# Performance work log

Hardware: AMD Instinct MI355X
Metric: run time of the kernel (lower is better)

## Reference

```python
import jax, jax.numpy as jnp
import numpy as np

B, S, H, NH, L, INTER, WIN = 2, 2048, 512, 8, 4, 2048, 64
HD = H // NH
W1 = WIN // 2          # one-sided window
WB = 2 * W1 + 1        # band width per query
EPS = 1e-12


def layer_norm(x, g, b):
    m = jnp.mean(x, axis=-1, keepdims=True)
    v = jnp.var(x, axis=-1, keepdims=True)
    return (x - m) / jnp.sqrt(v + EPS) * g + b


def setup_inputs() -> dict:
    key = jax.random.key(0)
    ks = jax.random.split(key, 12)
    std = 0.02
    n = lambda k, sh: jax.random.normal(k, sh, jnp.float32) * std
    return {
        "input_embs": jax.random.normal(ks[0], (B, S, H), jnp.float32),
        "attention_mask": jnp.ones((B, S), jnp.float32),
        "pos_emb": n(ks[1], (S, H)),
        "ln_emb_g": jnp.ones((H,), jnp.float32),
        "ln_emb_b": jnp.zeros((H,), jnp.float32),
        "Wq": n(ks[2], (L, H, H)), "bq": jnp.zeros((L, H), jnp.float32),
        "Wk": n(ks[3], (L, H, H)), "bk": jnp.zeros((L, H), jnp.float32),
        "Wv": n(ks[4], (L, H, H)), "bv": jnp.zeros((L, H), jnp.float32),
        "Wo": n(ks[5], (L, H, H)), "bo": jnp.zeros((L, H), jnp.float32),
        "ln1_g": jnp.ones((L, H), jnp.float32), "ln1_b": jnp.zeros((L, H), jnp.float32),
        "Wi": n(ks[6], (L, H, INTER)), "bi": jnp.zeros((L, INTER), jnp.float32),
        "Wo2": n(ks[7], (L, INTER, H)), "bo2": jnp.zeros((L, H), jnp.float32),
        "ln2_g": jnp.ones((L, H), jnp.float32), "ln2_b": jnp.zeros((L, H), jnp.float32),
        "pool_W1": n(ks[8], (H, H)), "pool_b1": jnp.zeros((H,), jnp.float32),
        "pool_W2": n(ks[9], (H, 1)), "pool_b2": jnp.zeros((1,), jnp.float32),
    }


def reference(input_embs, attention_mask, pos_emb, ln_emb_g, ln_emb_b,
              Wq, bq, Wk, bk, Wv, bv, Wo, bo, ln1_g, ln1_b,
              Wi, bi, Wo2, bo2, ln2_g, ln2_b,
              pool_W1, pool_b1, pool_W2, pool_b2):
    # extended additive mask: 0 for attend, -10000 for pad (no global tokens)
    ext = (1.0 - attention_mask) * -10000.0          # [B,S]
    is_masked = ext < 0                              # masked query positions

    # embeddings: input + position, LayerNorm (dropout is identity in eval)
    x = layer_norm(input_embs + pos_emb[None], ln_emb_g, ln_emb_b)

    # sliding-window band indices
    offs = jnp.arange(-W1, W1 + 1)
    idx = jnp.arange(S)[:, None] + offs[None, :]     # [S,WB]
    valid = (idx >= 0) & (idx < S)
    idxc = jnp.clip(idx, 0, S - 1)
    key_bias = ext[:, idxc]                          # [B,S,WB] additive key mask
    scale = 1.0 / jnp.sqrt(jnp.float32(HD))

    def layer(h, p):
        (wq, bq_, wk, bk_, wv, bv_, wo, bo_, g1, b1,
         wi, bi_, wo2, bo2_, g2, b2) = p
        q = (h @ wq + bq_).reshape(B, S, NH, HD) * scale
        k = (h @ wk + bk_).reshape(B, S, NH, HD)
        v = (h @ wv + bv_).reshape(B, S, NH, HD)
        kb = k[:, idxc]                              # [B,S,WB,NH,HD]
        vb = v[:, idxc]
        sc = jnp.einsum('bshd,bswhd->bhsw', q, kb) + key_bias[:, None]
        sc = jnp.where(valid[None, None], sc, -jnp.inf)
        pr = jax.nn.softmax(sc, axis=-1)
        pr = jnp.where(is_masked[:, None, :, None], 0.0, pr)
        ctx = jnp.einsum('bhsw,bswhd->bshd', pr, vb).reshape(B, S, H)
        attn = layer_norm(ctx @ wo + bo_ + h, g1, b1)          # BertSelfOutput
        inter = jax.nn.gelu(attn @ wi + bi_, approximate=False)  # BertIntermediate
        out = layer_norm(inter @ wo2 + bo2_ + attn, g2, b2)      # BertOutput
        return out, None

    params = (Wq, bq, Wk, bk, Wv, bv, Wo, bo, ln1_g, ln1_b,
              Wi, bi, Wo2, bo2, ln2_g, ln2_b)
    x, _ = jax.lax.scan(jax.checkpoint(layer), x, params)

    # AttentionPooling
    e = jnp.tanh(x @ pool_W1 + pool_b1)
    alpha = jnp.exp(e @ pool_W2 + pool_b2) * attention_mask[..., None]  # [B,S,1]
    alpha = alpha / (jnp.sum(alpha, axis=1, keepdims=True) + 1e-8)
    return jnp.einsum('bsh,bs->bh', x, alpha[..., 0])  # [B,H]
```

## Files before the change

kernel.cpp:

```cpp
#include <hip/hip_runtime.h>
#include <hip/hip_bf16.h>
#include <math.h>

#define B_ 2
#define S_ 2048
#define H_ 512
#define NH_ 8
#define HD_ 64
#define L_ 4
#define INTER_ 2048
#define W1_ 32
#define WB_ 65
#define M_ (B_*S_)

typedef __attribute__((ext_vector_type(8))) short short8v;
typedef __attribute__((ext_vector_type(4))) float f32x4;

__device__ __forceinline__ float b2f(ushort u){ return __uint_as_float(((unsigned)u)<<16); }
__device__ __forceinline__ ushort f2b(float f){
  unsigned u = __float_as_uint(f);
  unsigned r = (u + 0x7fffu + ((u>>16)&1u)) >> 16;
  return (ushort)r;
}

__device__ __forceinline__ void async16(const ushort* g, ushort* l){
  __builtin_amdgcn_global_load_lds(
      (const __attribute__((address_space(1))) unsigned int*)g,
      (__attribute__((address_space(3))) unsigned int*)l, 16, 0, 0);
}

__global__ __launch_bounds__(256) void transpose_k(const float* __restrict__ src,
    ushort* __restrict__ dst, int R, int C, size_t sBatch, size_t dBatch)
{
  __shared__ ushort tile[32][33];
  src += (size_t)blockIdx.z * sBatch;
  dst += (size_t)blockIdx.z * dBatch;
  int tx = threadIdx.x & 31, ty = threadIdx.x >> 5;
  int r0 = blockIdx.y * 32, c0 = blockIdx.x * 32;
  #pragma unroll
  for (int i = 0; i < 4; ++i){
    int r = r0 + ty + i*8;
    tile[ty + i*8][tx] = f2b(src[(size_t)r * C + c0 + tx]);
  }
  __syncthreads();
  #pragma unroll
  for (int i = 0; i < 4; ++i){
    int c = c0 + ty + i*8;
    dst[(size_t)c * R + r0 + tx] = tile[tx][ty + i*8];
  }
}

__global__ __launch_bounds__(256) void pack_bqkv(const float* __restrict__ bq,
    const float* __restrict__ bk, const float* __restrict__ bv, float* __restrict__ dst)
{
  int i = blockIdx.x * 256 + threadIdx.x;
  int l = i / 1536, n = i % 1536;
  float v = (n < 512) ? bq[l*512 + n] : (n < 1024 ? bk[l*512 + n - 512] : bv[l*512 + n - 1024]);
  dst[i] = v;
}

template<int EPI, int BM>
__global__ __launch_bounds__(256, (BM == 64) ? 4 : 3) void gemm_bt(
    const ushort* __restrict__ A, const ushort* __restrict__ Bt,
    const float* __restrict__ bias, ushort* __restrict__ o16,
    float* __restrict__ o32, int M, int N, int K, int Klen)
{
  constexpr int ABUF = BM * 32;
  constexpr int BUFE = ABUF + 4096;
  constexpr int MI = BM / 32;
  constexpr int AL = BM / 64;
  __shared__ ushort lds[3 * BUFE];
  const int tid = threadIdx.x;
  const int bm = blockIdx.y * BM, bn = blockIdx.x * 128;
  const int kbeg = blockIdx.z * Klen;
  const int wave = tid >> 6, lane = tid & 63;
  const int wr = (wave >> 1) * (BM / 2), wc = (wave & 1) * 64;
  const int lr = lane & 15, lg = lane >> 4;
  const int lkS = (lg ^ ((lr >> 1) & 3)) * 8;
  f32x4 acc[MI][4] = {};

  const int srow = tid >> 2;
  const int schk = (((tid & 3) ^ ((tid >> 3) & 3))) * 8;
  const ushort* Ag  = A  + (size_t)(bm + srow) * K + kbeg + schk;
  const ushort* Bg0 = Bt + (size_t)(bn + srow) * K + kbeg + schk;
  const ushort* Bg1 = Bt + (size_t)(bn + 64 + srow) * K + kbeg + schk;

  const int nIter = Klen >> 5;
  auto issueTile = [&](int t, int buf){
    int k0 = t << 5;
    ushort* d = &lds[0] + buf*BUFE + tid*8;
    #pragma unroll
    for (int r = 0; r < AL; ++r)
      async16(Ag + (size_t)r*64*K + k0, d + r*2048);
    async16(Bg0 + k0, d + ABUF);
    async16(Bg1 + k0, d + ABUF + 2048);
  };

  issueTile(0, 0);
  issueTile(1, 1);

  int cb = 0;
  for (int t = 0; t < nIter; ++t){
    int ib = cb + 2; if (ib >= 3) ib -= 3;
    if (t + 2 < nIter) issueTile(t + 2, ib);
    if constexpr (BM == 64){
      if (t + 2 < nIter)      asm volatile("s_waitcnt vmcnt(6)" ::: "memory");
      else if (t + 1 < nIter) asm volatile("s_waitcnt vmcnt(3)" ::: "memory");
      else                    asm volatile("s_waitcnt vmcnt(0)" ::: "memory");
    } else {
      if (t + 2 < nIter)      asm volatile("s_waitcnt vmcnt(8)" ::: "memory");
      else if (t + 1 < nIter) asm volatile("s_waitcnt vmcnt(4)" ::: "memory");
      else                    asm volatile("s_waitcnt vmcnt(0)" ::: "memory");
    }
    __builtin_amdgcn_sched_barrier(0);
    __builtin_amdgcn_s_barrier();
    const ushort* bufp = &lds[0] + cb*BUFE;
    short8v af[MI], bfr[4];
    #pragma unroll
    for (int mi = 0; mi < MI; ++mi)
      af[mi] = *(const short8v*)(bufp + (wr + mi*16 + lr)*32 + lkS);
    #pragma unroll
    for (int nj = 0; nj < 4; ++nj)
      bfr[nj] = *(const short8v*)(bufp + ABUF + (wc + nj*16 + lr)*32 + lkS);
    #pragma unroll
    for (int mi = 0; mi < MI; ++mi)
      #pragma unroll
      for (int nj = 0; nj < 4; ++nj)
        acc[mi][nj] = __builtin_amdgcn_mfma_f32_16x16x32_bf16(af[mi], bfr[nj], acc[mi][nj], 0, 0, 0);
    __builtin_amdgcn_s_barrier();
    cb = cb + 1; if (cb == 3) cb = 0;
  }

  const float bscale = (blockIdx.z == 0) ? 1.0f : 0.0f;
  #pragma unroll
  for (int mi = 0; mi < MI; ++mi){
    #pragma unroll
    for (int nj = 0; nj < 4; ++nj){
      int col = bn + wc + nj*16 + lr;
      float bv = bias[col] * bscale;
      #pragma unroll
      for (int j = 0; j < 4; ++j){
        int row = bm + wr + mi*16 + lg*4 + j;
        float v = acc[mi][nj][j] + bv;
        if (EPI == 1) v = 0.5f * v * (1.0f + erff(v * 0.70710678118654752f));
        if (EPI == 2) v = tanhf(v);
        if (EPI == 3) o32[(size_t)blockIdx.z*M*N + (size_t)row * N + col] = v;
        else          o16[(size_t)row * N + col] = f2b(v);
      }
    }
  }
}

__device__ __forceinline__ void block_ln_stats(float v0, float v1, float* red,
                                               float& mean, float& rstd)
{
  int tid = threadIdx.x, wave = tid >> 6, lane = tid & 63;
  float sm = v0 + v1;
  float sq = v0*v0 + v1*v1;
  #pragma unroll
  for (int o = 32; o > 0; o >>= 1){ sm += __shfl_xor(sm, o); sq += __shfl_xor(sq, o); }
  if (lane == 0){ red[wave] = sm; red[4 + wave] = sq; }
  __syncthreads();
  float S = red[0] + red[1] + red[2] + red[3];
  float Q = red[4] + red[5] + red[6] + red[7];
  mean = S * (1.0f / 512.0f);
  float var = Q * (1.0f / 512.0f) - mean*mean;
  if (var < 0.f) var = 0.f;
  rstd = rsqrtf(var + 1e-12f);
}

__global__ __launch_bounds__(256) void embed_ln(const float* __restrict__ x,
    const float* __restrict__ pos, const float* __restrict__ g,
    const float* __restrict__ bb, ushort* __restrict__ out16, float* __restrict__ out32)
{
  __shared__ float red[8];
  int row = blockIdx.x, tid = threadIdx.x;
  int s = row & (S_ - 1);
  const size_t base = (size_t)row*H_ + tid*2;
  float2 xv = *(const float2*)(x + base);
  float2 pv = *(const float2*)(pos + (size_t)s*H_ + tid*2);
  float v0 = xv.x + pv.x, v1 = xv.y + pv.y;
  float mean, rstd;
  block_ln_stats(v0, v1, red, mean, rstd);
  float2 gv = *(const float2*)(g + tid*2);
  float2 bv = *(const float2*)(bb + tid*2);
  float r0 = (v0 - mean)*rstd*gv.x + bv.x;
  float r1 = (v1 - mean)*rstd*gv.y + bv.y;
  ushort2 o2; o2.x = f2b(r0); o2.y = f2b(r1);
  *(ushort2*)(out16 + base) = o2;
  float2 f2v; f2v.x = r0; f2v.y = r1;
  *(float2*)(out32 + base) = f2v;
}

__global__ __launch_bounds__(256) void ln_res(const float* __restrict__ t,
    const float* __restrict__ res, const float* __restrict__ g,
    const float* __restrict__ bb, ushort* __restrict__ out16, float* __restrict__ out32)
{
  __shared__ float red[8];
  int row = blockIdx.x, tid = threadIdx.x;
  const size_t MN = (size_t)M_*H_;
  const size_t base = (size_t)row*H_ + tid*2;
  float2 t0 = *(const float2*)(t + base);
  float2 t1v = *(const float2*)(t + MN + base);
  float2 rv = *(const float2*)(res + base);
  float v0 = t0.x + t1v.x + rv.x;
  float v1 = t0.y + t1v.y + rv.y;
  float mean, rstd;
  block_ln_stats(v0, v1, red, mean, rstd);
  float2 gv = *(const float2*)(g + tid*2);
  float2 bv = *(const float2*)(bb + tid*2);
  float r0 = (v0 - mean)*rstd*gv.x + bv.x;
  float r1 = (v1 - mean)*rstd*gv.y + bv.y;
  ushort2 o2; o2.x = f2b(r0); o2.y = f2b(r1);
  *(ushort2*)(out16 + base) = o2;
  float2 f2v; f2v.x = r0; f2v.y = r1;
  *(float2*)(out32 + base) = f2v;
}

__global__ __launch_bounds__(256) void attn_mfma(const ushort* __restrict__ qkv,
    const float* __restrict__ mask, ushort* __restrict__ ctx)
{
  __shared__ ushort K_lds[128][72];
  __shared__ ushort Vt[64][136];
  __shared__ ushort P_lds[64][136];
  __shared__ float  kb[128];

  const int tid = threadIdx.x, wave = tid >> 6, lane = tid & 63;
  const int hh = blockIdx.y & (NH_ - 1), b = blockIdx.y >> 3;
  const int s0 = blockIdx.x * 64;
  const size_t rb = (size_t)b * S_;

  const int ch = tid & 7;
  const int rr = tid >> 3;
  #pragma unroll
  for (int it = 0; it < 4; ++it){
    int c = rr + it*32;
    int j = s0 - 32 + c;
    int jc = min(max(j, 0), S_ - 1);
    const size_t rowb = (rb + jc) * 1536 + hh*64 + ch*8;
    *(short8v*)(&K_lds[c][ch*8]) = *(const short8v*)(qkv + rowb + 512);
    short8v vv = *(const short8v*)(qkv + rowb + 1024);
    #pragma unroll
    for (int t = 0; t < 8; ++t){
      int tt = (t + ch) & 7;
      Vt[ch*8 + tt][c] = (ushort)vv[tt];
    }
  }
  if (tid < 128){
    int j = s0 - 32 + tid;
    kb[tid] = (j >= 0 && j < S_) ? (1.0f - mask[rb + j]) * (-10000.0f) : -1e30f;
  }
  __syncthreads();

  const int wq0 = wave * 16;
  const int lr = lane & 15, lg = lane >> 4, lk = lg * 8;

  const ushort* qbase = qkv + (rb + s0 + wq0 + lr) * 1536 + hh*64;
  short8v aq0 = *(const short8v*)(qbase + lk);
  short8v aq1 = *(const short8v*)(qbase + 32 + lk);

  f32x4 sacc[8];
  #pragma unroll
  for (int cn = 0; cn < 8; ++cn){
    short8v bk0 = *(const short8v*)(&K_lds[cn*16 + lr][lk]);
    short8v bk1 = *(const short8v*)(&K_lds[cn*16 + lr][32 + lk]);
    f32x4 z = {0.f, 0.f, 0.f, 0.f};
    z = __builtin_amdgcn_mfma_f32_16x16x32_bf16(aq0, bk0, z, 0, 0, 0);
    z = __builtin_amdgcn_mfma_f32_16x16x32_bf16(aq1, bk1, z, 0, 0, 0);
    sacc[cn] = z;
  }

  #pragma unroll
  for (int jr = 0; jr < 4; ++jr){
    const int R = wq0 + lg*4 + jr;
    float v[8], mx = -1e30f;
    #pragma unroll
    for (int cn = 0; cn < 8; ++cn){
      int c = cn*16 + lr;
      float sc = sacc[cn][jr] * 0.125f + kb[c];
      if (c < R || c > R + 64) sc = -1e30f;
      v[cn] = sc;
      mx = fmaxf(mx, sc);
    }
    #pragma unroll
    for (int o = 1; o < 16; o <<= 1) mx = fmaxf(mx, __shfl_xor(mx, o));
    float sum = 0.f;
    #pragma unroll
    for (int cn = 0; cn < 8; ++cn){ v[cn] = __expf(v[cn] - mx); sum += v[cn]; }
    #pragma unroll
    for (int o = 1; o < 16; o <<= 1) sum += __shfl_xor(sum, o);
    float qm = mask[rb + s0 + R];
    float inv = ((qm < 0.999f) ? 0.0f : 1.0f) / sum;
    #pragma unroll
    for (int cn = 0; cn < 8; ++cn)
      P_lds[R][cn*16 + lr] = f2b(v[cn] * inv);
  }

  short8v ap[4];
  #pragma unroll
  for (int ks = 0; ks < 4; ++ks)
    ap[ks] = *(const short8v*)(&P_lds[wq0 + lr][ks*32 + lk]);
  #pragma unroll
  for (int dn = 0; dn < 4; ++dn){
    f32x4 z = {0.f, 0.f, 0.f, 0.f};
    #pragma unroll
    for (int ks = 0; ks < 4; ++ks){
      short8v bv = *(const short8v*)(&Vt[dn*16 + lr][ks*32 + lk]);
      z = __builtin_amdgcn_mfma_f32_16x16x32_bf16(ap[ks], bv, z, 0, 0, 0);
    }
    #pragma unroll
    for (int jr = 0; jr < 4; ++jr){
      int R = wq0 + lg*4 + jr;
      ctx[(rb + s0 + R)*H_ + hh*64 + dn*16 + lr] = f2b(z[jr]);
    }
  }
}

__global__ __launch_bounds__(256) void pool_logit(const ushort* __restrict__ e,
    const float* __restrict__ w2, const float* __restrict__ b2p,
    const float* __restrict__ mask, float* __restrict__ alpha)
{
  int tid = threadIdx.x, wave = tid >> 6, lane = tid & 63;
  int r = blockIdx.x * 4 + wave;
  short8v ev = *(const short8v*)(e + (size_t)r*H_ + lane*8);
  float sacc = 0.f;
  #pragma unroll
  for (int j = 0; j < 8; ++j) sacc += b2f((ushort)ev[j]) * w2[lane*8 + j];
  #pragma unroll
  for (int o = 32; o > 0; o >>= 1) sacc += __shfl_xor(sacc, o);
  if (lane == 0){
    float logit = sacc + b2p[0];
    alpha[r] = __expf(logit) * mask[r];
  }
}

__global__ __launch_bounds__(256) void pool_sum(const float* __restrict__ alpha,
                                                float* __restrict__ invsum)
{
  __shared__ float red[4];
  int b = blockIdx.x, tid = threadIdx.x, wave = tid >> 6, lane = tid & 63;
  float s = 0.f;
  for (int k = tid; k < S_; k += 256) s += alpha[b*S_ + k];
  #pragma unroll
  for (int o = 32; o > 0; o >>= 1) s += __shfl_xor(s, o);
  if (lane == 0) red[wave] = s;
  __syncthreads();
  if (tid == 0) invsum[b] = 1.0f / (red[0] + red[1] + red[2] + red[3] + 1e-8f);
}

__global__ __launch_bounds__(256) void pool_wsum(const float* __restrict__ x,
    const float* __restrict__ alpha, float* __restrict__ out_acc)
{
  int chunk = blockIdx.x, b = blockIdx.y, tid = threadIdx.x;
  int s0 = chunk * 128;
  int c0 = tid * 2;
  float a0 = 0.f, a1 = 0.f;
  for (int i = 0; i < 128; ++i){
    int srow = s0 + i;
    float al = alpha[b*S_ + srow];
    float2 xv = *(const float2*)(x + (size_t)(b*S_ + srow)*H_ + c0);
    a0 += xv.x * al;
    a1 += xv.y * al;
  }
  float2 o; o.x = a0; o.y = a1;
  *(float2*)(out_acc + (size_t)chunk*B_*H_ + b*H_ + c0) = o;
}

__global__ __launch_bounds__(256) void pool_final(const float* __restrict__ out_acc,
    const float* __restrict__ invsum, float* __restrict__ out)
{
  int i = blockIdx.x * 256 + threadIdx.x;
  if (i < B_*H_){
    int b = i >> 9;
    float s = 0.f;
    #pragma unroll
    for (int c = 0; c < 16; ++c) s += out_acc[(size_t)c*B_*H_ + i];
    out[i] = s * invsum[b];
  }
}

extern "C" void kernel_launch(void* const* d_in, const int* in_sizes, int n_in,
                              void* d_out, int out_size, void* d_ws, size_t ws_size,
                              hipStream_t stream)
{
  const float* input_embs = (const float*)d_in[0];
  const float* mask       = (const float*)d_in[1];
  const float* pos        = (const float*)d_in[2];
  const float* ln_emb_g   = (const float*)d_in[3];
  const float* ln_emb_b   = (const float*)d_in[4];
  const float* Wq  = (const float*)d_in[5];
  const float* bq  = (const float*)d_in[6];
  const float* Wk  = (const float*)d_in[7];
  const float* bk  = (const float*)d_in[8];
  const float* Wv  = (const float*)d_in[9];
  const float* bv  = (const float*)d_in[10];
  const float* Wo  = (const float*)d_in[11];
  const float* bo  = (const float*)d_in[12];
  const float* ln1_g = (const float*)d_in[13];
  const float* ln1_b = (const float*)d_in[14];
  const float* Wi  = (const float*)d_in[15];
  const float* bi  = (const float*)d_in[16];
  const float* Wo2 = (const float*)d_in[17];
  const float* bo2 = (const float*)d_in[18];
  const float* ln2_g = (const float*)d_in[19];
  const float* ln2_b = (const float*)d_in[20];
  const float* pW1 = (const float*)d_in[21];
  const float* pb1 = (const float*)d_in[22];
  const float* pW2 = (const float*)d_in[23];
  const float* pb2 = (const float*)d_in[24];

  char* ws = (char*)d_ws;
  size_t off = 0;
  auto alloc = [&](size_t bytes)->char*{
    char* p = ws + off; off += (bytes + 255) & ~(size_t)255; return p;
  };
  ushort* WqkvT  = (ushort*)alloc((size_t)L_*1536*512*2);
  ushort* WoT    = (ushort*)alloc((size_t)L_*512*512*2);
  ushort* WiT    = (ushort*)alloc((size_t)L_*2048*512*2);
  ushort* Wo2T   = (ushort*)alloc((size_t)L_*512*2048*2);
  ushort* pW1T   = (ushort*)alloc((size_t)512*512*2);
  float*  bqkv   = (float*)alloc((size_t)L_*1536*4);
  ushort* h16    = (ushort*)alloc((size_t)M_*H_*2);
  float*  h32    = (float*)alloc((size_t)M_*H_*4);
  ushort* qkv    = (ushort*)alloc((size_t)M_*1536*2);
  ushort* ctx    = (ushort*)alloc((size_t)M_*H_*2);
  ushort* attn16 = (ushort*)alloc((size_t)M_*H_*2);
  float*  attn32 = (float*)alloc((size_t)M_*H_*4);
  ushort* inter  = (ushort*)alloc((size_t)M_*INTER_*2);
  float*  t1     = (float*)alloc((size_t)2*M_*H_*4);
  float*  alpha  = (float*)alloc((size_t)M_*4);
  float*  invsum = (float*)alloc(256);
  float*  outacc = (float*)alloc((size_t)16*B_*H_*4);

  dim3 tb(256);
  transpose_k<<<dim3(16,16,L_), tb, 0, stream>>>(Wq, WqkvT,            512,  512, (size_t)512*512,  (size_t)1536*512);
  transpose_k<<<dim3(16,16,L_), tb, 0, stream>>>(Wk, WqkvT + 512*512,  512,  512, (size_t)512*512,  (size_t)1536*512);
  transpose_k<<<dim3(16,16,L_), tb, 0, stream>>>(Wv, WqkvT + 1024*512, 512,  512, (size_t)512*512,  (size_t)1536*512);
  transpose_k<<<dim3(16,16,L_), tb, 0, stream>>>(Wo, WoT,              512,  512, (size_t)512*512,  (size_t)512*512);
  transpose_k<<<dim3(64,16,L_), tb, 0, stream>>>(Wi, WiT,              512, 2048, (size_t)512*2048, (size_t)2048*512);
  transpose_k<<<dim3(16,64,L_), tb, 0, stream>>>(Wo2, Wo2T,           2048,  512, (size_t)2048*512, (size_t)512*2048);
  transpose_k<<<dim3(16,16,1),  tb, 0, stream>>>(pW1, pW1T,            512,  512, 0, 0);
  pack_bqkv<<<dim3(L_*1536/256), tb, 0, stream>>>(bq, bk, bv, bqkv);

  embed_ln<<<dim3(M_), tb, 0, stream>>>(input_embs, pos, ln_emb_g, ln_emb_b, h16, h32);

  for (int l = 0; l < L_; ++l){
    gemm_bt<0,128><<<dim3(12,32,1), tb, 0, stream>>>(h16, WqkvT + (size_t)l*1536*512, bqkv + l*1536,
                                                     qkv, nullptr, M_, 1536, 512, 512);
    attn_mfma<<<dim3(S_/64, B_*NH_), tb, 0, stream>>>(qkv, mask, ctx);
    gemm_bt<3,64><<<dim3(4,64,2), tb, 0, stream>>>(ctx, WoT + (size_t)l*512*512, bo + l*512,
                                                   nullptr, t1, M_, 512, 512, 256);
    ln_res<<<dim3(M_), tb, 0, stream>>>(t1, h32, ln1_g + l*512, ln1_b + l*512, attn16, attn32);
    gemm_bt<1,128><<<dim3(16,32,1), tb, 0, stream>>>(attn16, WiT + (size_t)l*2048*512, bi + l*2048,
                                                     inter, nullptr, M_, 2048, 512, 512);
    gemm_bt<3,64><<<dim3(4,64,2), tb, 0, stream>>>(inter, Wo2T + (size_t)l*512*2048, bo2 + l*512,
                                                   nullptr, t1, M_, 512, 2048, 1024);
    ln_res<<<dim3(M_), tb, 0, stream>>>(t1, attn32, ln2_g + l*512, ln2_b + l*512, h16, h32);
  }

  gemm_bt<2,64><<<dim3(4,64,1), tb, 0, stream>>>(h16, pW1T, pb1, ctx, nullptr, M_, 512, 512, 512);
  pool_logit<<<dim3(M_/4), tb, 0, stream>>>(ctx, pW2, pb2, mask, alpha);
  pool_sum<<<dim3(B_), tb, 0, stream>>>(alpha, invsum);
  pool_wsum<<<dim3(16, B_), tb, 0, stream>>>(h32, alpha, outacc);
  pool_final<<<dim3((B_*H_ + 255)/256), tb, 0, stream>>>(outacc, invsum, (float*)d_out);
}
```

Measured before the change: 411.0 us.

## Merge 512x512 weight transposes, pack V transpose stores, shrink QKV GEMM tile

```diff
diff --git a/kernel.cpp b/kernel.cpp
--- a/kernel.cpp
+++ b/kernel.cpp
@@ -29,14 +29,11 @@
       (__attribute__((address_space(3))) unsigned int*)l, 16, 0, 0);
 }
 
-__global__ __launch_bounds__(256) void transpose_k(const float* __restrict__ src,
-    ushort* __restrict__ dst, int R, int C, size_t sBatch, size_t dBatch)
+__device__ __forceinline__ void tr_tile(const float* __restrict__ src,
+    ushort* __restrict__ dst, int R, int C, int r0, int c0)
 {
   __shared__ ushort tile[32][33];
-  src += (size_t)blockIdx.z * sBatch;
-  dst += (size_t)blockIdx.z * dBatch;
   int tx = threadIdx.x & 31, ty = threadIdx.x >> 5;
-  int r0 = blockIdx.y * 32, c0 = blockIdx.x * 32;
   #pragma unroll
   for (int i = 0; i < 4; ++i){
     int r = r0 + ty + i*8;
@@ -48,6 +45,39 @@
     int c = c0 + ty + i*8;
     dst[(size_t)c * R + r0 + tx] = tile[tx][ty + i*8];
   }
+}
+
+struct TPack {
+  const float* wq; const float* wk; const float* wv;
+  const float* wo; const float* pw1;
+  ushort* wqkvT; ushort* woT; ushort* pw1T;
+};
+
+__global__ __launch_bounds__(256) void transpose512_all(TPack p)
+{
+  int z = blockIdx.z;
+  const float* src; ushort* dst;
+  if (z < 12){
+    int kind = z >> 2, l = z & 3;
+    const float* s3[3] = {p.wq, p.wk, p.wv};
+    src = s3[kind] + (size_t)l*512*512;
+    dst = p.wqkvT + (size_t)l*1536*512 + (size_t)kind*512*512;
+  } else if (z < 16){
+    int l = z - 12;
+    src = p.wo + (size_t)l*512*512;
+    dst = p.woT + (size_t)l*512*512;
+  } else {
+    src = p.pw1; dst = p.pw1T;
+  }
+  tr_tile(src, dst, 512, 512, blockIdx.y*32, blockIdx.x*32);
+}
+
+__global__ __launch_bounds__(256) void transpose_k(const float* __restrict__ src,
+    ushort* __restrict__ dst, int R, int C, size_t sBatch, size_t dBatch)
+{
+  src += (size_t)blockIdx.z * sBatch;
+  dst += (size_t)blockIdx.z * dBatch;
+  tr_tile(src, dst, R, C, blockIdx.y*32, blockIdx.x*32);
 }
 
 __global__ __launch_bounds__(256) void pack_bqkv(const float* __restrict__ bq,
@@ -233,17 +263,24 @@
   const int ch = tid & 7;
   const int rr = tid >> 3;
   #pragma unroll
-  for (int it = 0; it < 4; ++it){
-    int c = rr + it*32;
-    int j = s0 - 32 + c;
-    int jc = min(max(j, 0), S_ - 1);
-    const size_t rowb = (rb + jc) * 1536 + hh*64 + ch*8;
-    *(short8v*)(&K_lds[c][ch*8]) = *(const short8v*)(qkv + rowb + 512);
-    short8v vv = *(const short8v*)(qkv + rowb + 1024);
+  for (int it = 0; it < 2; ++it){
+    int c0 = rr*2 + it*64;
+    short8v vv[2];
+    #pragma unroll
+    for (int p = 0; p < 2; ++p){
+      int c = c0 + p;
+      int j = s0 - 32 + c;
+      int jc = min(max(j, 0), S_ - 1);
+      const size_t rowb = (rb + jc) * 1536 + hh*64 + ch*8;
+      *(short8v*)(&K_lds[c][ch*8]) = *(const short8v*)(qkv + rowb + 512);
+      vv[p] = *(const short8v*)(qkv + rowb + 1024);
+    }
     #pragma unroll
     for (int t = 0; t < 8; ++t){
       int tt = (t + ch) & 7;
-      Vt[ch*8 + tt][c] = (ushort)vv[tt];
+      int d = ch*8 + tt;
+      ushort2 w; w.x = (ushort)vv[0][tt]; w.y = (ushort)vv[1][tt];
+      *(ushort2*)(&Vt[d][c0]) = w;
     }
   }
   if (tid < 128){
@@ -433,20 +470,19 @@
   float*  outacc = (float*)alloc((size_t)16*B_*H_*4);
 
   dim3 tb(256);
-  transpose_k<<<dim3(16,16,L_), tb, 0, stream>>>(Wq, WqkvT,            512,  512, (size_t)512*512,  (size_t)1536*512);
-  transpose_k<<<dim3(16,16,L_), tb, 0, stream>>>(Wk, WqkvT + 512*512,  512,  512, (size_t)512*512,  (size_t)1536*512);
-  transpose_k<<<dim3(16,16,L_), tb, 0, stream>>>(Wv, WqkvT + 1024*512, 512,  512, (size_t)512*512,  (size_t)1536*512);
-  transpose_k<<<dim3(16,16,L_), tb, 0, stream>>>(Wo, WoT,              512,  512, (size_t)512*512,  (size_t)512*512);
-  transpose_k<<<dim3(64,16,L_), tb, 0, stream>>>(Wi, WiT,              512, 2048, (size_t)512*2048, (size_t)2048*512);
-  transpose_k<<<dim3(16,64,L_), tb, 0, stream>>>(Wo2, Wo2T,           2048,  512, (size_t)2048*512, (size_t)512*2048);
-  transpose_k<<<dim3(16,16,1),  tb, 0, stream>>>(pW1, pW1T,            512,  512, 0, 0);
+  TPack tp;
+  tp.wq = Wq; tp.wk = Wk; tp.wv = Wv; tp.wo = Wo; tp.pw1 = pW1;
+  tp.wqkvT = WqkvT; tp.woT = WoT; tp.pw1T = pW1T;
+  transpose512_all<<<dim3(16,16,17), tb, 0, stream>>>(tp);
+  transpose_k<<<dim3(64,16,L_), tb, 0, stream>>>(Wi, WiT,    512, 2048, (size_t)512*2048, (size_t)2048*512);
+  transpose_k<<<dim3(16,64,L_), tb, 0, stream>>>(Wo2, Wo2T, 2048,  512, (size_t)2048*512, (size_t)512*2048);
   pack_bqkv<<<dim3(L_*1536/256), tb, 0, stream>>>(bq, bk, bv, bqkv);
 
   embed_ln<<<dim3(M_), tb, 0, stream>>>(input_embs, pos, ln_emb_g, ln_emb_b, h16, h32);
 
   for (int l = 0; l < L_; ++l){
-    gemm_bt<0,128><<<dim3(12,32,1), tb, 0, stream>>>(h16, WqkvT + (size_t)l*1536*512, bqkv + l*1536,
-                                                     qkv, nullptr, M_, 1536, 512, 512);
+    gemm_bt<0,64><<<dim3(12,64,1), tb, 0, stream>>>(h16, WqkvT + (size_t)l*1536*512, bqkv + l*1536,
+                                                    qkv, nullptr, M_, 1536, 512, 512);
     attn_mfma<<<dim3(S_/64, B_*NH_), tb, 0, stream>>>(qkv, mask, ctx);
     gemm_bt<3,64><<<dim3(4,64,2), tb, 0, stream>>>(ctx, WoT + (size_t)l*512*512, bo + l*512,
                                                    nullptr, t1, M_, 512, 512, 256);
```

Result: no change. 403.6 us (-1.8%).
